# Performance work log

Measured on AMD Instinct MI355X. Metric: run time of the kernel, lower is better.

## Reference

```python
import math
import jax, jax.numpy as jnp
import numpy as np

B, W_LEN, C = 4, 2048, 768
H = 3  # fixed number of heads in the module
K = C // H  # head dim


def setup_inputs() -> dict:
    key = jax.random.key(0)
    k1, k2, k3 = jax.random.split(key, 3)
    in_sequence_bwc = jax.random.normal(k1, (B, W_LEN, C), dtype=jnp.float32)
    # torch nn.Linear weights: [out_features, in_features], scaled for stability
    W_qkv = jax.random.normal(k2, (3 * C, C), dtype=jnp.float32) * (1.0 / math.sqrt(C))
    W_proj = jax.random.normal(k3, (C, C), dtype=jnp.float32) * (1.0 / math.sqrt(C))
    return {"in_sequence_bwc": in_sequence_bwc, "W_qkv": W_qkv, "W_proj": W_proj}


def reference(in_sequence_bwc, W_qkv, W_proj):
    batch, words, coords = in_sequence_bwc.shape
    head_dim = coords // H
    # qkv projection: x @ W^T  -> [b, w, 3c]
    all_bwd = jnp.einsum("bwc,dc->bwd", in_sequence_bwc, W_qkv)
    q_bwc, k_bwc, v_bwc = jnp.split(all_bwd, 3, axis=-1)
    # [b, h, w, k]
    q = q_bwc.reshape(batch, words, H, head_dim).transpose(0, 2, 1, 3)
    k = k_bwc.reshape(batch, words, H, head_dim).transpose(0, 2, 1, 3)
    v = v_bwc.reshape(batch, words, H, head_dim).transpose(0, 2, 1, 3)
    # scaled scores with causal mask -> softmax -> @V
    scores = jnp.einsum("bhqk,bhmk->bhqm", q, k) / math.sqrt(head_dim)
    causal = jnp.tril(jnp.ones((words, words), dtype=bool))
    scores = jnp.where(causal[None, None], scores, -jnp.inf)
    probs = jax.nn.softmax(scores, axis=-1)
    out = jnp.einsum("bhqm,bhmk->bhqk", probs, v)
    out_bwc = out.transpose(0, 2, 1, 3).reshape(batch, words, coords)
    return jnp.einsum("bwc,dc->bwd", out_bwc, W_proj)
```

## Files before the change

kernel.cpp:

```cpp
#include <hip/hip_runtime.h>

using v8h = __attribute__((ext_vector_type(8))) _Float16;
using v4f = __attribute__((ext_vector_type(4))) float;
using v4u = __attribute__((ext_vector_type(4))) unsigned short;
using v8u = __attribute__((ext_vector_type(8))) unsigned short;

__device__ __forceinline__ unsigned short f2h(float x) {
  _Float16 h = (_Float16)x;
  return __builtin_bit_cast(unsigned short, h);
}
__device__ __forceinline__ float h2f(unsigned short u) {
  return (float)__builtin_bit_cast(_Float16, u);
}

__device__ __forceinline__ void gl_lds16(const unsigned short* g, unsigned short* l) {
  __builtin_amdgcn_global_load_lds(
      (const __attribute__((address_space(1))) unsigned int*)g,
      (__attribute__((address_space(3))) unsigned int*)l, 16, 0, 0);
}

__global__ void cvt_kernel(const float* __restrict__ src,
                           unsigned short* __restrict__ dst, int n8) {
  int i = blockIdx.x * 256 + threadIdx.x;
  if (i >= n8) return;
  const float* p = src + (size_t)i * 8;
  float4 a = *(const float4*)p;
  float4 b = *(const float4*)(p + 4);
  v8u o = {f2h(a.x), f2h(a.y), f2h(a.z), f2h(a.w),
           f2h(b.x), f2h(b.y), f2h(b.z), f2h(b.w)};
  *(v8u*)(dst + (size_t)i * 8) = o;
}

__global__ __launch_bounds__(512, 2)
void qkv8_kernel(const unsigned short* __restrict__ A,
                 const unsigned short* __restrict__ Bw,
                 unsigned short* __restrict__ QK,
                 unsigned short* __restrict__ VT) {
  __shared__ unsigned short sm[65536];
  const int t    = (int)threadIdx.x;
  const int ln   = t & 63;
  const int wv   = t >> 6;
  const int quad = ln >> 4;
  const int L    = ln & 15;
  const int wm   = wv >> 2;
  const int wn   = wv & 3;
  const long m0  = (long)blockIdx.y * 256;
  const long n0  = (long)blockIdx.x * 256;

  const int srow = t >> 3;
  const int scol = ((t & 7) ^ (srow & 7)) * 8;
  const unsigned short* Ath = A + (m0 + srow) * 768 + scol;
  const unsigned short* Bth = Bw + (n0 + srow) * 768 + scol;
  unsigned short* lth = &sm[t * 8];

  const int l7   = L & 7;
  const int sl0  = ((0 + quad) ^ l7) * 8;
  const int sl1  = ((4 + quad) ^ l7) * 8;
  const int arow = (wm * 128 + L) * 64;
  const int brow = (wn * 64 + L) * 64;

  v4f acc[8][4];
#pragma unroll
  for (int i = 0; i < 8; i++)
#pragma unroll
    for (int j = 0; j < 4; j++) acc[i][j] = (v4f){0.f, 0.f, 0.f, 0.f};

  auto stA = [&](int tile, int h) {
    if (tile >= 12) return;
    const unsigned short* g = Ath + (h * 128) * 768 + tile * 64;
    unsigned short* l = lth + (tile & 1) * 32768 + h * 8192;
    gl_lds16(g, l);
    gl_lds16(g + 64 * 768, l + 4096);
  };
  auto stB = [&](int tile, int h) {
    if (tile >= 12) return;
    const unsigned short* g = Bth + (h * 128) * 768 + tile * 64;
    unsigned short* l = lth + (tile & 1) * 32768 + 16384 + h * 8192;
    gl_lds16(g, l);
    gl_lds16(g + 64 * 768, l + 4096);
  };

  stB(0, 0); stB(0, 1); stA(0, 0); stA(0, 1);
  stB(1, 0); stB(1, 1); stA(1, 0);
  asm volatile("s_waitcnt vmcnt(6)" ::: "memory");
  __builtin_amdgcn_s_barrier();
  __builtin_amdgcn_sched_barrier(0);

#pragma unroll 2
  for (int kt = 0; kt < 12; ++kt) {
    const unsigned short* sA = &sm[(kt & 1) * 32768];
    const unsigned short* sB = sA + 16384;
    v8h af[4][2], b0[2][2], b1[2][2];

#pragma unroll
    for (int i = 0; i < 4; i++) {
      af[i][0] = *(const v8h*)&sA[arow + i * 1024 + sl0];
      af[i][1] = *(const v8h*)&sA[arow + i * 1024 + sl1];
    }
#pragma unroll
    for (int j = 0; j < 2; j++) {
      b0[j][0] = *(const v8h*)&sB[brow + j * 1024 + sl0];
      b0[j][1] = *(const v8h*)&sB[brow + j * 1024 + sl1];
    }
    stA(kt + 1, 1);
    __builtin_amdgcn_s_barrier();
    asm volatile("s_waitcnt lgkmcnt(0)" ::: "memory");
    __builtin_amdgcn_sched_barrier(0);
    __builtin_amdgcn_s_setprio(1);
#pragma unroll
    for (int i = 0; i < 4; i++)
#pragma unroll
      for (int j = 0; j < 2; j++) {
        acc[i][j] = __builtin_amdgcn_mfma_f32_16x16x32_f16(af[i][0], b0[j][0], acc[i][j], 0, 0, 0);
        acc[i][j] = __builtin_amdgcn_mfma_f32_16x16x32_f16(af[i][1], b0[j][1], acc[i][j], 0, 0, 0);
      }
    __builtin_amdgcn_s_setprio(0);
    __builtin_amdgcn_s_barrier();
    __builtin_amdgcn_sched_barrier(0);

#pragma unroll
    for (int j = 0; j < 2; j++) {
      b1[j][0] = *(const v8h*)&sB[brow + 2048 + j * 1024 + sl0];
      b1[j][1] = *(const v8h*)&sB[brow + 2048 + j * 1024 + sl1];
    }
    __builtin_amdgcn_s_barrier();
    asm volatile("s_waitcnt lgkmcnt(0)" ::: "memory");
    __builtin_amdgcn_sched_barrier(0);
    __builtin_amdgcn_s_setprio(1);
#pragma unroll
    for (int i = 0; i < 4; i++)
#pragma unroll
      for (int j = 0; j < 2; j++) {
        acc[i][2 + j] = __builtin_amdgcn_mfma_f32_16x16x32_f16(af[i][0], b1[j][0], acc[i][2 + j], 0, 0, 0);
        acc[i][2 + j] = __builtin_amdgcn_mfma_f32_16x16x32_f16(af[i][1], b1[j][1], acc[i][2 + j], 0, 0, 0);
      }
    __builtin_amdgcn_s_setprio(0);
    __builtin_amdgcn_s_barrier();
    __builtin_amdgcn_sched_barrier(0);

#pragma unroll
    for (int i = 0; i < 4; i++) {
      af[i][0] = *(const v8h*)&sA[arow + 4096 + i * 1024 + sl0];
      af[i][1] = *(const v8h*)&sA[arow + 4096 + i * 1024 + sl1];
    }
    stB(kt + 2, 0);
    __builtin_amdgcn_s_barrier();
    asm volatile("s_waitcnt lgkmcnt(0)" ::: "memory");
    __builtin_amdgcn_sched_barrier(0);
    __builtin_amdgcn_s_setprio(1);
#pragma unroll
    for (int i = 0; i < 4; i++)
#pragma unroll
      for (int j = 0; j < 2; j++) {
        acc[4 + i][2 + j] = __builtin_amdgcn_mfma_f32_16x16x32_f16(af[i][0], b1[j][0], acc[4 + i][2 + j], 0, 0, 0);
        acc[4 + i][2 + j] = __builtin_amdgcn_mfma_f32_16x16x32_f16(af[i][1], b1[j][1], acc[4 + i][2 + j], 0, 0, 0);
      }
    __builtin_amdgcn_s_setprio(0);
    __builtin_amdgcn_s_barrier();
    __builtin_amdgcn_sched_barrier(0);

    stB(kt + 2, 1);
    stA(kt + 2, 0);
    __builtin_amdgcn_s_barrier();
    __builtin_amdgcn_sched_barrier(0);
    __builtin_amdgcn_s_setprio(1);
#pragma unroll
    for (int i = 0; i < 4; i++)
#pragma unroll
      for (int j = 0; j < 2; j++) {
        acc[4 + i][j] = __builtin_amdgcn_mfma_f32_16x16x32_f16(af[i][0], b0[j][0], acc[4 + i][j], 0, 0, 0);
        acc[4 + i][j] = __builtin_amdgcn_mfma_f32_16x16x32_f16(af[i][1], b0[j][1], acc[4 + i][j], 0, 0, 0);
      }
    __builtin_amdgcn_s_setprio(0);
    if (kt + 2 < 12)      { asm volatile("s_waitcnt vmcnt(6)" ::: "memory"); }
    else if (kt + 1 < 12) { asm volatile("s_waitcnt vmcnt(0)" ::: "memory"); }
    __builtin_amdgcn_s_barrier();
    __builtin_amdgcn_sched_barrier(0);
  }

  if (n0 < 1536) {
#pragma unroll
    for (int mi = 0; mi < 8; mi++) {
      const long row = m0 + wm * 128 + (mi >> 2) * 64 + (mi & 3) * 16 + quad * 4;
#pragma unroll
      for (int nj = 0; nj < 4; nj++) {
        const long col = n0 + wn * 64 + nj * 16 + L;
#pragma unroll
        for (int r = 0; r < 4; r++)
          QK[(row + r) * 1536 + col] = f2h(acc[mi][nj][r]);
      }
    }
  } else {
#pragma unroll
    for (int mi = 0; mi < 8; mi++) {
      const long token = m0 + wm * 128 + (mi >> 2) * 64 + (mi & 3) * 16 + quad * 4;
      const int b  = (int)(token >> 11);
      const int tk = (int)(token & 2047);
#pragma unroll
      for (int nj = 0; nj < 4; nj++) {
        const int colp = (int)(n0 + wn * 64 + nj * 16 + L) - 1536;
        const int h = colp >> 8;
        const int d = colp & 255;
        v4u val = {f2h(acc[mi][nj][0]), f2h(acc[mi][nj][1]),
                   f2h(acc[mi][nj][2]), f2h(acc[mi][nj][3])};
        *(v4u*)(&VT[((long)(b * 3 + h) * 256 + d) * 2048 + tk]) = val;
      }
    }
  }
}

template <int MODE, bool OF>
__global__ __launch_bounds__(256, 2)
void gemm_async_kernel(const unsigned short* __restrict__ A,
                       const unsigned short* __restrict__ Bw,
                       void* __restrict__ Cv, unsigned short* __restrict__ VT,
                       int K, int ldc) {
  __shared__ unsigned short As[4096];
  __shared__ unsigned short Bs[4096];

  const int t    = threadIdx.x;
  const int ln   = t & 63;
  const int wv   = t >> 6;
  const int quad = ln >> 4;
  const int L    = ln & 15;
  const int wm   = (wv >> 1) * 64;
  const int wn   = (wv & 1) * 64;
  const long m0  = (long)blockIdx.y * 128;
  const long n0  = (long)blockIdx.x * 128;

  v4f acc[4][4];
#pragma unroll
  for (int i = 0; i < 4; i++)
#pragma unroll
    for (int j = 0; j < 4; j++) acc[i][j] = (v4f){0.f, 0.f, 0.f, 0.f};

  const int ar = t >> 2;
  const int ac = (t & 3) * 8;
  const unsigned short* Ag = A + (m0 + ar) * (long)K + ac;
  const unsigned short* Bg = Bw + (n0 + ar) * (long)K + ac;
  unsigned short* la = &As[t * 8];
  unsigned short* lb = &Bs[t * 8];
  const long rowskip = 64L * K;

  for (int k0 = 0; k0 < K; k0 += 32) {
    gl_lds16(Ag + k0, la);
    gl_lds16(Ag + rowskip + k0, la + 2048);
    gl_lds16(Bg + k0, lb);
    gl_lds16(Bg + rowskip + k0, lb + 2048);
    __syncthreads();

    v8h af[4], bfr[4];
#pragma unroll
    for (int i = 0; i < 4; i++)
      af[i] = *(const v8h*)(&As[(wm + i * 16 + L) * 32 + quad * 8]);
#pragma unroll
    for (int j = 0; j < 4; j++)
      bfr[j] = *(const v8h*)(&Bs[(wn + j * 16 + L) * 32 + quad * 8]);
#pragma unroll
    for (int i = 0; i < 4; i++)
#pragma unroll
      for (int j = 0; j < 4; j++)
        acc[i][j] = __builtin_amdgcn_mfma_f32_16x16x32_f16(af[i], bfr[j], acc[i][j], 0, 0, 0);
    __syncthreads();
  }

  if (MODE == 0 || n0 < 1536) {
#pragma unroll
    for (int i = 0; i < 4; i++)
#pragma unroll
      for (int j = 0; j < 4; j++)
#pragma unroll
        for (int r = 0; r < 4; r++) {
          long row = m0 + wm + i * 16 + quad * 4 + r;
          long col = n0 + wn + j * 16 + L;
          if (OF) ((float*)Cv)[row * ldc + col] = acc[i][j][r];
          else    ((unsigned short*)Cv)[row * ldc + col] = f2h(acc[i][j][r]);
        }
  } else {
#pragma unroll
    for (int i = 0; i < 4; i++)
#pragma unroll
      for (int j = 0; j < 4; j++) {
        int colp   = (int)(n0 + wn + j * 16 + L) - 1536;
        int h      = colp >> 8;
        int d      = colp & 255;
        long token = m0 + wm + i * 16 + quad * 4;
        int b  = (int)(token >> 11);
        int tk = (int)(token & 2047);
        v4u val = {f2h(acc[i][j][0]), f2h(acc[i][j][1]), f2h(acc[i][j][2]), f2h(acc[i][j][3])};
        *(v4u*)(&VT[((long)(b * 3 + h) * 256 + d) * 2048 + tk]) = val;
      }
  }
}

__global__ __launch_bounds__(256, 2)
void gemm_sc_kernel(const unsigned short* __restrict__ QK,
                    unsigned short* __restrict__ Sc) {
  __shared__ unsigned short As[4096];
  __shared__ unsigned short Bs[4096];

  const int t    = threadIdx.x;
  const int ln   = t & 63;
  const int wv   = t >> 6;
  const int quad = ln >> 4;
  const int L    = ln & 15;
  const int wm   = (wv >> 1) * 64;
  const int wn   = (wv & 1) * 64;

  int x = (int)blockIdx.x, i = 0;
  while (x >= i + 1) { x -= i + 1; i++; }
  const int j  = x;
  const int bh = (int)blockIdx.y;
  const int b  = bh / 3, h = bh % 3;
  const long tokA = (long)b * 2048 + i * 128;
  const long tokB = (long)b * 2048 + j * 128;

  v4f acc[4][4];
#pragma unroll
  for (int ii = 0; ii < 4; ii++)
#pragma unroll
    for (int jj = 0; jj < 4; jj++) acc[ii][jj] = (v4f){0.f, 0.f, 0.f, 0.f};

  const int ar = t >> 2;
  const int ac = (t & 3) * 8;
  const unsigned short* Ag = QK + (tokA + ar) * 1536 + h * 256 + ac;
  const unsigned short* Bg = QK + (tokB + ar) * 1536 + 768 + h * 256 + ac;
  unsigned short* la = &As[t * 8];
  unsigned short* lb = &Bs[t * 8];
  const long rowskip = 64L * 1536;

  for (int k0 = 0; k0 < 256; k0 += 32) {
    gl_lds16(Ag + k0, la);
    gl_lds16(Ag + rowskip + k0, la + 2048);
    gl_lds16(Bg + k0, lb);
    gl_lds16(Bg + rowskip + k0, lb + 2048);
    __syncthreads();

    v8h af[4], bfr[4];
#pragma unroll
    for (int ii = 0; ii < 4; ii++)
      af[ii] = *(const v8h*)(&As[(wm + ii * 16 + L) * 32 + quad * 8]);
#pragma unroll
    for (int jj = 0; jj < 4; jj++)
      bfr[jj] = *(const v8h*)(&Bs[(wn + jj * 16 + L) * 32 + quad * 8]);
#pragma unroll
    for (int ii = 0; ii < 4; ii++)
#pragma unroll
      for (int jj = 0; jj < 4; jj++)
        acc[ii][jj] = __builtin_amdgcn_mfma_f32_16x16x32_f16(af[ii], bfr[jj], acc[ii][jj], 0, 0, 0);
    __syncthreads();
  }

  unsigned short* Sb = Sc + ((long)bh * 136 + blockIdx.x) * 16384;
#pragma unroll
  for (int ii = 0; ii < 4; ii++)
#pragma unroll
    for (int jj = 0; jj < 4; jj++)
#pragma unroll
      for (int r = 0; r < 4; r++) {
        int row = wm + ii * 16 + quad * 4 + r;
        int col = wn + jj * 16 + L;
        Sb[row * 128 + col] = f2h(acc[ii][jj][r]);
      }
}

__global__ __launch_bounds__(256, 4)
void softmax_kernel(unsigned short* __restrict__ Sc) {
  const int tt   = threadIdx.x;
  const int wv   = tt >> 6;
  const int lane = tt & 63;
  const int bh   = (int)blockIdx.y;

  const int r = 2047 - ((int)blockIdx.x * 4 + wv);
  const int i = r >> 7;
  const int rowloc = r & 127;
  const long base = ((long)bh * 136 + (long)i * (i + 1) / 2) * 16384 + rowloc * 128;
  const int Lrow = (i + 1) * 128;
  const int nch = (i + 4) >> 2;

  float xs[4][8];
  float mx = -1e30f;
  for (int k = 0; k < nch; k++) {
    int c0 = k * 512 + lane * 8;
    if (c0 < Lrow) {
      int j = c0 >> 7;
      v8u v = *(const v8u*)(Sc + base + (long)j * 16384 + (c0 & 127));
#pragma unroll
      for (int e = 0; e < 8; e++) {
        float f = (c0 + e <= r) ? h2f(v[e]) * 0.0625f : -1e30f;
        xs[k][e] = f;
        mx = fmaxf(mx, f);
      }
    } else {
#pragma unroll
      for (int e = 0; e < 8; e++) xs[k][e] = -1e30f;
    }
  }
#pragma unroll
  for (int d = 1; d < 64; d <<= 1) mx = fmaxf(mx, __shfl_xor(mx, d));

  float sum = 0.f;
  for (int k = 0; k < nch; k++)
#pragma unroll
    for (int e = 0; e < 8; e++) {
      float ex = __expf(xs[k][e] - mx);
      xs[k][e] = ex;
      sum += ex;
    }
#pragma unroll
  for (int d = 1; d < 64; d <<= 1) sum += __shfl_xor(sum, d);
  const float inv = 1.0f / sum;

  for (int k = 0; k < nch; k++) {
    int c0 = k * 512 + lane * 8;
    if (c0 < Lrow) {
      int j = c0 >> 7;
      v8u o;
#pragma unroll
      for (int e = 0; e < 8; e++) o[e] = f2h(xs[k][e] * inv);
      *(v8u*)(Sc + base + (long)j * 16384 + (c0 & 127)) = o;
    }
  }
}

__global__ __launch_bounds__(256, 2)
void gemm_pv_kernel(const unsigned short* __restrict__ Sc,
                    const unsigned short* __restrict__ VT,
                    unsigned short* __restrict__ Pp) {
  __shared__ unsigned short As[4096];
  __shared__ unsigned short Bs[4096];

  const int t    = threadIdx.x;
  const int ln   = t & 63;
  const int wv   = t >> 6;
  const int quad = ln >> 4;
  const int L    = ln & 15;
  const int wm   = (wv >> 1) * 64;
  const int wn   = (wv & 1) * 64;

  const int ix  = (int)blockIdx.x;
  const int i   = 15 - (ix >> 2);
  const int nh  = (ix >> 1) & 1;
  const int par = ix & 1;
  const int bh  = (int)blockIdx.y;

  v4f acc[4][4];
#pragma unroll
  for (int ii = 0; ii < 4; ii++)
#pragma unroll
    for (int jj = 0; jj < 4; jj++) acc[ii][jj] = (v4f){0.f, 0.f, 0.f, 0.f};

  const int ar = t >> 2;
  const int ac = (t & 3) * 8;
  const unsigned short* Abase =
      Sc + ((long)bh * 136 + (long)i * (i + 1) / 2) * 16384 + ar * 128 + ac;
  const unsigned short* Bg =
      VT + ((long)bh * 256 + nh * 128 + ar) * 2048 + ac;
  unsigned short* la = &As[t * 8];
  unsigned short* lb = &Bs[t * 8];

  for (int j = par; j <= i; j += 2) {
    const unsigned short* Aj = Abase + (long)j * 16384;
    const unsigned short* Bj = Bg + j * 128;
#pragma unroll
    for (int k0 = 0; k0 < 128; k0 += 32) {
      gl_lds16(Aj + k0, la);
      gl_lds16(Aj + 64 * 128 + k0, la + 2048);
      gl_lds16(Bj + k0, lb);
      gl_lds16(Bj + 64 * 2048 + k0, lb + 2048);
      __syncthreads();

      v8h af[4], bfr[4];
#pragma unroll
      for (int ii = 0; ii < 4; ii++)
        af[ii] = *(const v8h*)(&As[(wm + ii * 16 + L) * 32 + quad * 8]);
#pragma unroll
      for (int jj = 0; jj < 4; jj++)
        bfr[jj] = *(const v8h*)(&Bs[(wn + jj * 16 + L) * 32 + quad * 8]);
#pragma unroll
      for (int ii = 0; ii < 4; ii++)
#pragma unroll
        for (int jj = 0; jj < 4; jj++)
          acc[ii][jj] = __builtin_amdgcn_mfma_f32_16x16x32_f16(af[ii], bfr[jj], acc[ii][jj], 0, 0, 0);
      __syncthreads();
    }
  }

  unsigned short* Pb = Pp + ((((long)bh * 16 + i) * 2 + nh) * 2 + par) * 16384;
#pragma unroll
  for (int ii = 0; ii < 4; ii++)
#pragma unroll
    for (int jj = 0; jj < 4; jj++)
#pragma unroll
      for (int r = 0; r < 4; r++) {
        int row = wm + ii * 16 + quad * 4 + r;
        int col = wn + jj * 16 + L;
        Pb[row * 128 + col] = f2h(acc[ii][jj][r]);
      }
}

__global__ __launch_bounds__(256, 4)
void pv_combine_kernel(const unsigned short* __restrict__ Pp,
                       unsigned short* __restrict__ AO) {
  const int i  = (int)blockIdx.x >> 1;
  const int nh = (int)blockIdx.x & 1;
  const int bh = (int)blockIdx.y;
  const int b  = bh / 3, h = bh % 3;

  const int tid = threadIdx.x;
  const int row = tid >> 1;
  const int cs  = (tid & 1) * 64;

  const unsigned short* P0 = Pp + ((((long)bh * 16 + i) * 2 + nh) * 2 + 0) * 16384 + row * 128 + cs;
  const unsigned short* P1 = P0 + 16384;
  unsigned short* Or = AO + ((long)b * 2048 + i * 128 + row) * 768 + h * 256 + nh * 128 + cs;
#pragma unroll
  for (int q = 0; q < 8; q++) {
    v8u a = *(const v8u*)(P0 + q * 8);
    v8u c = *(const v8u*)(P1 + q * 8);
    v8u o;
#pragma unroll
    for (int e = 0; e < 8; e++) o[e] = f2h(h2f(a[e]) + h2f(c[e]));
    *(v8u*)(Or + q * 8) = o;
  }
}

extern "C" void kernel_launch(void* const* d_in, const int* in_sizes, int n_in,
                              void* d_out, int out_size, void* d_ws, size_t ws_size,
                              hipStream_t stream) {
  const float* X     = (const float*)d_in[0];
  const float* Wqkv  = (const float*)d_in[1];
  const float* Wproj = (const float*)d_in[2];
  float* out = (float*)d_out;

  const size_t SZ_QK = (size_t)8192 * 1536 * 2;
  const size_t SZ_VT = (size_t)3072 * 2048 * 2;
  const size_t SZ_SC = (size_t)12 * 136 * 16384 * 2;
  const size_t SZ_AO = (size_t)8192 * 768 * 2;
  const size_t SZ_WQ = (size_t)2304 * 768 * 2;

  char* ws = (char*)d_ws;
  unsigned short* QKb = (unsigned short*)ws;
  unsigned short* Ppb = QKb;
  unsigned short* VTb = (unsigned short*)(ws + SZ_QK);
  unsigned short* Scb = (unsigned short*)(ws + SZ_QK + SZ_VT);
  unsigned short* Xb  = Scb;
  unsigned short* AOb = (unsigned short*)(ws + SZ_QK + SZ_VT + SZ_SC);
  unsigned short* Wqb = (unsigned short*)(ws + SZ_QK + SZ_VT + SZ_SC + SZ_AO);
  unsigned short* Wpb = (unsigned short*)(ws + SZ_QK + SZ_VT + SZ_SC + SZ_AO + SZ_WQ);

  dim3 blk(256, 1, 1);
  cvt_kernel<<<dim3(3072, 1, 1), blk, 0, stream>>>(X, Xb, 786432);
  cvt_kernel<<<dim3(864, 1, 1), blk, 0, stream>>>(Wqkv, Wqb, 221184);
  cvt_kernel<<<dim3(288, 1, 1), blk, 0, stream>>>(Wproj, Wpb, 73728);
  qkv8_kernel<<<dim3(9, 32, 1), dim3(512, 1, 1), 0, stream>>>(Xb, Wqb, QKb, VTb);
  gemm_sc_kernel<<<dim3(136, 12, 1), blk, 0, stream>>>(QKb, Scb);
  softmax_kernel<<<dim3(512, 12, 1), blk, 0, stream>>>(Scb);
  gemm_pv_kernel<<<dim3(64, 12, 1), blk, 0, stream>>>(Scb, VTb, Ppb);
  pv_combine_kernel<<<dim3(32, 12, 1), blk, 0, stream>>>(Ppb, AOb);
  gemm_async_kernel<0, true><<<dim3(6, 64, 1), blk, 0, stream>>>(
      AOb, Wpb, out, (unsigned short*)nullptr, 768, 768);
}
```

Baseline: 265.6 us.

## Move V projection into score kernel and merge the three conversion launches

The V-part of the QKV projection is removed from the big qkv8 GEMM, which now covers only the Q and K columns. Those V tiles are computed as extra blocks of the score GEMM launch, so they fill idle slots left by the triangular causal tile count. The three fp32-to-fp16 conversion launches are merged into one kernel. Xb is moved to the AO buffer so it does not overlap the score buffer. The V blocks use the simpler 128x128 GEMM with a K loop of 768, which is less efficient than the tuned qkv8 kernel, and the load imbalance between block types may grow.

```diff
diff --git a/kernel.cpp b/kernel.cpp
--- a/kernel.cpp
+++ b/kernel.cpp
@@ -19,10 +19,19 @@
       (__attribute__((address_space(3))) unsigned int*)l, 16, 0, 0);
 }
 
-__global__ void cvt_kernel(const float* __restrict__ src,
-                           unsigned short* __restrict__ dst, int n8) {
-  int i = blockIdx.x * 256 + threadIdx.x;
-  if (i >= n8) return;
+__global__ void cvt3_kernel(const float* __restrict__ X,
+                            const float* __restrict__ Wq,
+                            const float* __restrict__ Wp,
+                            unsigned short* __restrict__ Xb,
+                            unsigned short* __restrict__ Wqb,
+                            unsigned short* __restrict__ Wpb) {
+  const int blk = (int)blockIdx.x;
+  const float* src;
+  unsigned short* dst;
+  int i;
+  if (blk < 3072)      { src = X;  dst = Xb;  i = blk * 256 + threadIdx.x; }
+  else if (blk < 3936) { src = Wq; dst = Wqb; i = (blk - 3072) * 256 + threadIdx.x; }
+  else                 { src = Wp; dst = Wpb; i = (blk - 3936) * 256 + threadIdx.x; }
   const float* p = src + (size_t)i * 8;
   float4 a = *(const float4*)p;
   float4 b = *(const float4*)(p + 4);
@@ -34,8 +43,7 @@
 __global__ __launch_bounds__(512, 2)
 void qkv8_kernel(const unsigned short* __restrict__ A,
                  const unsigned short* __restrict__ Bw,
-                 unsigned short* __restrict__ QK,
-                 unsigned short* __restrict__ VT) {
+                 unsigned short* __restrict__ QK) {
   __shared__ unsigned short sm[65536];
   const int t    = (int)threadIdx.x;
   const int ln   = t & 63;
@@ -178,43 +186,23 @@
     __builtin_amdgcn_sched_barrier(0);
   }
 
-  if (n0 < 1536) {
-#pragma unroll
-    for (int mi = 0; mi < 8; mi++) {
-      const long row = m0 + wm * 128 + (mi >> 2) * 64 + (mi & 3) * 16 + quad * 4;
-#pragma unroll
-      for (int nj = 0; nj < 4; nj++) {
-        const long col = n0 + wn * 64 + nj * 16 + L;
-#pragma unroll
-        for (int r = 0; r < 4; r++)
-          QK[(row + r) * 1536 + col] = f2h(acc[mi][nj][r]);
-      }
-    }
-  } else {
-#pragma unroll
-    for (int mi = 0; mi < 8; mi++) {
-      const long token = m0 + wm * 128 + (mi >> 2) * 64 + (mi & 3) * 16 + quad * 4;
-      const int b  = (int)(token >> 11);
-      const int tk = (int)(token & 2047);
-#pragma unroll
-      for (int nj = 0; nj < 4; nj++) {
-        const int colp = (int)(n0 + wn * 64 + nj * 16 + L) - 1536;
-        const int h = colp >> 8;
-        const int d = colp & 255;
-        v4u val = {f2h(acc[mi][nj][0]), f2h(acc[mi][nj][1]),
-                   f2h(acc[mi][nj][2]), f2h(acc[mi][nj][3])};
-        *(v4u*)(&VT[((long)(b * 3 + h) * 256 + d) * 2048 + tk]) = val;
-      }
-    }
-  }
-}
-
-template <int MODE, bool OF>
+#pragma unroll
+  for (int mi = 0; mi < 8; mi++) {
+    const long row = m0 + wm * 128 + (mi >> 2) * 64 + (mi & 3) * 16 + quad * 4;
+#pragma unroll
+    for (int nj = 0; nj < 4; nj++) {
+      const long col = n0 + wn * 64 + nj * 16 + L;
+#pragma unroll
+      for (int r = 0; r < 4; r++)
+        QK[(row + r) * 1536 + col] = f2h(acc[mi][nj][r]);
+    }
+  }
+}
+
 __global__ __launch_bounds__(256, 2)
-void gemm_async_kernel(const unsigned short* __restrict__ A,
-                       const unsigned short* __restrict__ Bw,
-                       void* __restrict__ Cv, unsigned short* __restrict__ VT,
-                       int K, int ldc) {
+void gemm_proj_kernel(const unsigned short* __restrict__ A,
+                      const unsigned short* __restrict__ Bw,
+                      float* __restrict__ C) {
   __shared__ unsigned short As[4096];
   __shared__ unsigned short Bs[4096];
 
@@ -236,13 +224,13 @@
 
   const int ar = t >> 2;
   const int ac = (t & 3) * 8;
-  const unsigned short* Ag = A + (m0 + ar) * (long)K + ac;
-  const unsigned short* Bg = Bw + (n0 + ar) * (long)K + ac;
+  const unsigned short* Ag = A + (m0 + ar) * 768 + ac;
+  const unsigned short* Bg = Bw + (n0 + ar) * 768 + ac;
   unsigned short* la = &As[t * 8];
   unsigned short* lb = &Bs[t * 8];
-  const long rowskip = 64L * K;
-
-  for (int k0 = 0; k0 < K; k0 += 32) {
+  const long rowskip = 64L * 768;
+
+  for (int k0 = 0; k0 < 768; k0 += 32) {
     gl_lds16(Ag + k0, la);
     gl_lds16(Ag + rowskip + k0, la + 2048);
     gl_lds16(Bg + k0, lb);
@@ -264,38 +252,24 @@
     __syncthreads();
   }
 
-  if (MODE == 0 || n0 < 1536) {
-#pragma unroll
-    for (int i = 0; i < 4; i++)
-#pragma unroll
-      for (int j = 0; j < 4; j++)
-#pragma unroll
-        for (int r = 0; r < 4; r++) {
-          long row = m0 + wm + i * 16 + quad * 4 + r;
-          long col = n0 + wn + j * 16 + L;
-          if (OF) ((float*)Cv)[row * ldc + col] = acc[i][j][r];
-          else    ((unsigned short*)Cv)[row * ldc + col] = f2h(acc[i][j][r]);
-        }
-  } else {
-#pragma unroll
-    for (int i = 0; i < 4; i++)
-#pragma unroll
-      for (int j = 0; j < 4; j++) {
-        int colp   = (int)(n0 + wn + j * 16 + L) - 1536;
-        int h      = colp >> 8;
-        int d      = colp & 255;
-        long token = m0 + wm + i * 16 + quad * 4;
-        int b  = (int)(token >> 11);
-        int tk = (int)(token & 2047);
-        v4u val = {f2h(acc[i][j][0]), f2h(acc[i][j][1]), f2h(acc[i][j][2]), f2h(acc[i][j][3])};
-        *(v4u*)(&VT[((long)(b * 3 + h) * 256 + d) * 2048 + tk]) = val;
-      }
-  }
+#pragma unroll
+  for (int i = 0; i < 4; i++)
+#pragma unroll
+    for (int j = 0; j < 4; j++)
+#pragma unroll
+      for (int r = 0; r < 4; r++) {
+        long row = m0 + wm + i * 16 + quad * 4 + r;
+        long col = n0 + wn + j * 16 + L;
+        C[row * 768 + col] = acc[i][j][r];
+      }
 }
 
 __global__ __launch_bounds__(256, 2)
-void gemm_sc_kernel(const unsigned short* __restrict__ QK,
-                    unsigned short* __restrict__ Sc) {
+void scv_kernel(const unsigned short* __restrict__ QK,
+                const unsigned short* __restrict__ Xb,
+                const unsigned short* __restrict__ Wq,
+                unsigned short* __restrict__ Sc,
+                unsigned short* __restrict__ VT) {
   __shared__ unsigned short As[4096];
   __shared__ unsigned short Bs[4096];
 
@@ -306,14 +280,39 @@
   const int L    = ln & 15;
   const int wm   = (wv >> 1) * 64;
   const int wn   = (wv & 1) * 64;
-
-  int x = (int)blockIdx.x, i = 0;
-  while (x >= i + 1) { x -= i + 1; i++; }
-  const int j  = x;
+  const int ar   = t >> 2;
+  const int ac   = (t & 3) * 8;
+
+  const int x  = (int)blockIdx.x;
   const int bh = (int)blockIdx.y;
-  const int b  = bh / 3, h = bh % 3;
-  const long tokA = (long)b * 2048 + i * 128;
-  const long tokB = (long)b * 2048 + j * 128;
+  const bool isV = (x >= 136);
+
+  const unsigned short* Ag;
+  const unsigned short* Bg;
+  long rowstride;
+  int Klen;
+  int mt = 0, nt = 0;
+
+  if (!isV) {
+    int xx = x, i = 0;
+    while (xx >= i + 1) { xx -= i + 1; i++; }
+    const int j = xx;
+    const int b = bh / 3, h = bh % 3;
+    const long tokA = (long)b * 2048 + i * 128;
+    const long tokB = (long)b * 2048 + j * 128;
+    Ag = QK + (tokA + ar) * 1536 + h * 256 + ac;
+    Bg = QK + (tokB + ar) * 1536 + 768 + h * 256 + ac;
+    rowstride = 1536;
+    Klen = 256;
+  } else {
+    const int vi = (x - 136) + 32 * bh;
+    mt = vi & 63;
+    nt = vi >> 6;
+    Ag = Xb + ((long)mt * 128 + ar) * 768 + ac;
+    Bg = Wq + ((long)(1536 + nt * 128) + ar) * 768 + ac;
+    rowstride = 768;
+    Klen = 768;
+  }
 
   v4f acc[4][4];
 #pragma unroll
@@ -321,15 +320,11 @@
 #pragma unroll
     for (int jj = 0; jj < 4; jj++) acc[ii][jj] = (v4f){0.f, 0.f, 0.f, 0.f};
 
-  const int ar = t >> 2;
-  const int ac = (t & 3) * 8;
-  const unsigned short* Ag = QK + (tokA + ar) * 1536 + h * 256 + ac;
-  const unsigned short* Bg = QK + (tokB + ar) * 1536 + 768 + h * 256 + ac;
   unsigned short* la = &As[t * 8];
   unsigned short* lb = &Bs[t * 8];
-  const long rowskip = 64L * 1536;
-
-  for (int k0 = 0; k0 < 256; k0 += 32) {
+  const long rowskip = 64L * rowstride;
+
+  for (int k0 = 0; k0 < Klen; k0 += 32) {
     gl_lds16(Ag + k0, la);
     gl_lds16(Ag + rowskip + k0, la + 2048);
     gl_lds16(Bg + k0, lb);
@@ -351,17 +346,34 @@
     __syncthreads();
   }
 
-  unsigned short* Sb = Sc + ((long)bh * 136 + blockIdx.x) * 16384;
-#pragma unroll
-  for (int ii = 0; ii < 4; ii++)
-#pragma unroll
-    for (int jj = 0; jj < 4; jj++)
-#pragma unroll
-      for (int r = 0; r < 4; r++) {
-        int row = wm + ii * 16 + quad * 4 + r;
-        int col = wn + jj * 16 + L;
-        Sb[row * 128 + col] = f2h(acc[ii][jj][r]);
-      }
+  if (!isV) {
+    unsigned short* Sb = Sc + ((long)bh * 136 + x) * 16384;
+#pragma unroll
+    for (int ii = 0; ii < 4; ii++)
+#pragma unroll
+      for (int jj = 0; jj < 4; jj++)
+#pragma unroll
+        for (int r = 0; r < 4; r++) {
+          int row = wm + ii * 16 + quad * 4 + r;
+          int col = wn + jj * 16 + L;
+          Sb[row * 128 + col] = f2h(acc[ii][jj][r]);
+        }
+  } else {
+#pragma unroll
+    for (int ii = 0; ii < 4; ii++)
+#pragma unroll
+      for (int jj = 0; jj < 4; jj++) {
+        const int colp = nt * 128 + wn + jj * 16 + L;
+        const int h    = colp >> 8;
+        const int d    = colp & 255;
+        const long token = (long)mt * 128 + wm + ii * 16 + quad * 4;
+        const int b  = (int)(token >> 11);
+        const int tk = (int)(token & 2047);
+        v4u val = {f2h(acc[ii][jj][0]), f2h(acc[ii][jj][1]),
+                   f2h(acc[ii][jj][2]), f2h(acc[ii][jj][3])};
+        *(v4u*)(&VT[((long)(b * 3 + h) * 256 + d) * 2048 + tk]) = val;
+      }
+  }
 }
 
 __global__ __launch_bounds__(256, 4)
@@ -544,20 +556,17 @@
   unsigned short* Ppb = QKb;
   unsigned short* VTb = (unsigned short*)(ws + SZ_QK);
   unsigned short* Scb = (unsigned short*)(ws + SZ_QK + SZ_VT);
-  unsigned short* Xb  = Scb;
   unsigned short* AOb = (unsigned short*)(ws + SZ_QK + SZ_VT + SZ_SC);
+  unsigned short* Xb  = AOb;
   unsigned short* Wqb = (unsigned short*)(ws + SZ_QK + SZ_VT + SZ_SC + SZ_AO);
   unsigned short* Wpb = (unsigned short*)(ws + SZ_QK + SZ_VT + SZ_SC + SZ_AO + SZ_WQ);
 
   dim3 blk(256, 1, 1);
-  cvt_kernel<<<dim3(3072, 1, 1), blk, 0, stream>>>(X, Xb, 786432);
-  cvt_kernel<<<dim3(864, 1, 1), blk, 0, stream>>>(Wqkv, Wqb, 221184);
-  cvt_kernel<<<dim3(288, 1, 1), blk, 0, stream>>>(Wproj, Wpb, 73728);
-  qkv8_kernel<<<dim3(9, 32, 1), dim3(512, 1, 1), 0, stream>>>(Xb, Wqb, QKb, VTb);
-  gemm_sc_kernel<<<dim3(136, 12, 1), blk, 0, stream>>>(QKb, Scb);
+  cvt3_kernel<<<dim3(4224, 1, 1), blk, 0, stream>>>(X, Wqkv, Wproj, Xb, Wqb, Wpb);
+  qkv8_kernel<<<dim3(6, 32, 1), dim3(512, 1, 1), 0, stream>>>(Xb, Wqb, QKb);
+  scv_kernel<<<dim3(168, 12, 1), blk, 0, stream>>>(QKb, Xb, Wqb, Scb, VTb);
   softmax_kernel<<<dim3(512, 12, 1), blk, 0, stream>>>(Scb);
   gemm_pv_kernel<<<dim3(64, 12, 1), blk, 0, stream>>>(Scb, VTb, Ppb);
   pv_combine_kernel<<<dim3(32, 12, 1), blk, 0, stream>>>(Ppb, AOb);
-  gemm_async_kernel<0, true><<<dim3(6, 64, 1), blk, 0, stream>>>(
-      AOb, Wpb, out, (unsigned short*)nullptr, 768, 768);
-}
+  gemm_proj_kernel<<<dim3(6, 64, 1), blk, 0, stream>>>(AOb, Wpb, out);
+}
```

Result: faster. 257.1 us (-3.2%).
